# Kernel tuning notes

Measured on AMD Instinct MI355X. Metric: run time of the kernel, lower is better.

The kernel has to match this reference:

```python
import jax, jax.numpy as jnp
import numpy as np

NUM_EMBEDDINGS = 1024
EMBEDDING_DIM = 64
COMMITMENT_COST = 0.25


def setup_inputs() -> dict:
    key = jax.random.key(0)
    k1, k2 = jax.random.split(key)
    inputs = jax.random.normal(k1, (2, 64, 32, 32, 32), dtype=jnp.float32)
    embedding = jax.random.normal(k2, (NUM_EMBEDDINGS, EMBEDDING_DIM), dtype=jnp.float32)
    return {"inputs": inputs, "embedding": embedding}


def reference(inputs, embedding):
    # inputs: [B, C, D, H, W], embedding: [K, C]
    B, C, D, H, W = inputs.shape
    # flatten_permutation = [0, 2, 3, 4, 1] -> [B*D*H*W, C]
    flat_input = jnp.transpose(inputs, (0, 2, 3, 4, 1)).reshape(-1, C)
    # squared euclidean distances [N, K]
    distances = (
        jnp.sum(flat_input**2, axis=1, keepdims=True)
        + jnp.sum(embedding**2, axis=1)[None, :]
        - 2.0 * flat_input @ embedding.T
    )
    # torch.max(-distances, dim=1)[1] == argmin of distances
    encoding_indices = jnp.argmax(-distances, axis=1)  # [N]
    encoding_indices_view = encoding_indices.reshape(B, D, H, W)
    # embed: lookup then quantization_permutation [0, 4, 1, 2, 3] -> channel-first
    quantized = embedding[encoding_indices_view]            # [B, D, H, W, C]
    quantized = jnp.transpose(quantized, (0, 4, 1, 2, 3))   # [B, C, D, H, W]
    # commitment loss: MSE(stop_grad(quantized), inputs)
    loss = COMMITMENT_COST * jnp.mean((jax.lax.stop_gradient(quantized) - inputs) ** 2)
    # straight-through estimator
    quantized_st = inputs + jax.lax.stop_gradient(quantized - inputs)
    # eval path: encodings_sum = zeros(256) (hardcoded in original forward)
    encodings_sum = jnp.zeros(256, dtype=jnp.float32)
    return quantized_st, loss, encoding_indices_view, encodings_sum, embedding
```

## Files before the change

### kernel.cpp

```cpp
#include <hip/hip_runtime.h>
#include <stdint.h>

#define KCODES  1024
#define CDIM    64
#define SPATIAL 32768
#define NPOS    65536
#define NEL     4194304

#define OUT_Q    0
#define OUT_LOSS 4194304
#define OUT_IDX  4194305
#define OUT_SUM  4259841
#define OUT_EMB  4260097

#define NSET  32
#define SETB  8192
#define EIEXP 262144
#define BPOS  256

typedef _Float16 half8  __attribute__((ext_vector_type(8)));
typedef float    f32x4  __attribute__((ext_vector_type(4)));
typedef float    f32x16 __attribute__((ext_vector_type(16)));

__global__ void prep_emb(const float* __restrict__ emb, char* __restrict__ ws,
                         float* __restrict__ out) {
    int gt = blockIdx.x * 256 + threadIdx.x;
    if (gt == 0) out[OUT_LOSS] = 0.f;
    if (gt < 256) out[OUT_SUM + gt] = 0.f;
    {
        float4 v = *(const float4*)(emb + (size_t)gt * 4);
        float* o = out + OUT_EMB + (size_t)gt * 4;
        o[0] = v.x; o[1] = v.y; o[2] = v.z; o[3] = v.w;
    }
    if (gt < 8192) {
        int k = gt >> 3, oct = gt & 7;
        int set = k >> 5, row = k & 31;
        int ks = oct >> 1, hc = oct & 1;
        const float* e = emb + (size_t)k * CDIM + oct * 8;
        char* rec = ws + (size_t)set * SETB;
        _Float16* hi = (_Float16*)(rec + (ks * 2 + 0) * 1024 + (hc * 32 + row) * 16);
        _Float16* lo = (_Float16*)(rec + (ks * 2 + 1) * 1024 + (hc * 32 + row) * 16);
        float s2 = 0.f;
        half8 hv, lv;
#pragma unroll
        for (int i = 0; i < 8; ++i) {
            float v = e[i];
            s2 = fmaf(v, v, s2);
            _Float16 h = (_Float16)v;
            hv[i] = h;
            lv[i] = (_Float16)(v - (float)h);
        }
        *(half8*)hi = hv;
        *(half8*)lo = lv;
        s2 += __shfl_xor(s2, 1);
        s2 += __shfl_xor(s2, 2);
        s2 += __shfl_xor(s2, 4);
        if (oct == 0) {
            int hh = (row >> 2) & 1;
            int q  = (row & 3) | ((row >> 3) << 2);
            ((float*)(ws + EIEXP))[(set * 2 + hh) * 16 + q] = -0.5f * s2;
        }
    }
}

#define GLDS16(GSRC, LDST)                                                     \
    __builtin_amdgcn_global_load_lds(                                          \
        (const __attribute__((address_space(1))) void*)(GSRC),                 \
        (__attribute__((address_space(3))) void*)(LDST), 16, 0, 0)

__global__ __launch_bounds__(512, 2) void vq_kernel(
        const float* __restrict__ in, const float* __restrict__ emb,
        const char* __restrict__ wsA, float* __restrict__ out) {
    __shared__ __align__(16) char stg[3][SETB];
    __shared__ float xl[CDIM * 129];
    __shared__ __align__(16) float eiL[NSET * 32];
    __shared__ int   kwin[BPOS];
    __shared__ float lred[8];

    const int tid  = threadIdx.x;
    const int lane = tid & 63, wv = tid >> 6;
    const int col  = lane & 31, h = lane >> 5;
    const int p0   = blockIdx.x * BPOS;
    const int b    = p0 >> 15;
    const int s0   = p0 & 32767;
    const float* xin = in + (size_t)b * (CDIM * SPATIAL) + s0;
    const float* eiG = (const float*)(wsA + EIEXP);

    eiL[tid] = eiG[tid];
    eiL[tid + 512] = eiG[tid + 512];

    half8 bh[4], bl[4];
    for (int H = 0; H < 2; ++H) {
        {
            int p = tid & 127, cq = tid >> 7;
#pragma unroll
            for (int j = 0; j < 16; ++j) {
                int c = cq * 16 + j;
                xl[c * 129 + p] = xin[(size_t)c * SPATIAL + H * 128 + p];
            }
        }
        __syncthreads();
        if ((wv >> 2) == H) {
            int pp = (wv & 3) * 32 + col;
#pragma unroll
            for (int ks = 0; ks < 4; ++ks)
#pragma unroll
                for (int j = 0; j < 8; ++j) {
                    int c = ks * 16 + h * 8 + j;
                    float v = xl[c * 129 + pp];
                    _Float16 hh = (_Float16)v;
                    bh[ks][j] = hh;
                    bl[ks][j] = (_Float16)(v - (float)hh);
                }
        }
        __syncthreads();
    }

    GLDS16(wsA + 0 * SETB + wv * 1024 + lane * 16, &stg[0][0] + wv * 1024 + lane * 16);
    GLDS16(wsA + 1 * SETB + wv * 1024 + lane * 16, &stg[1][0] + wv * 1024 + lane * 16);

    float best = -3.402823466e38f;
    int   bk   = 0;
    char* cur = &stg[0][0];
    char* nxt = &stg[1][0];
    char* fut = &stg[2][0];
#pragma unroll 1
    for (int it = 0; it < NSET; ++it) {
        asm volatile("s_waitcnt vmcnt(1)" ::: "memory");
        __syncthreads();
        {
            int sN = (it + 2) & (NSET - 1);
            GLDS16(wsA + (size_t)sN * SETB + wv * 1024 + lane * 16,
                   fut + wv * 1024 + lane * 16);
        }
        f32x16 aA = *(const f32x16*)&eiL[(it * 2 + h) * 16];
        f32x16 aB, aC;
#pragma unroll
        for (int q = 0; q < 16; ++q) { aB[q] = 0.f; aC[q] = 0.f; }
        const char* ap = cur + (size_t)lane * 16;
#pragma unroll
        for (int ks = 0; ks < 4; ++ks) {
            half8 ah = *(const half8*)(ap + (ks * 2 + 0) * 1024);
            half8 al = *(const half8*)(ap + (ks * 2 + 1) * 1024);
            aA = __builtin_amdgcn_mfma_f32_32x32x16_f16(ah, bh[ks], aA, 0, 0, 0);
            aB = __builtin_amdgcn_mfma_f32_32x32x16_f16(ah, bl[ks], aB, 0, 0, 0);
            aC = __builtin_amdgcn_mfma_f32_32x32x16_f16(al, bh[ks], aC, 0, 0, 0);
        }
        const int kbase = it * 32 + 4 * h;
#pragma unroll
        for (int q = 0; q < 16; ++q) {
            float sc = (aA[q] + aB[q]) + aC[q];
            int   kk = kbase + (q & 3) + 8 * (q >> 2);
            if (sc > best) { best = sc; bk = kk; }
        }
        char* t0 = cur; cur = nxt; nxt = fut; fut = t0;
    }

    {
        float os = __shfl_xor(best, 32);
        int   ok = __shfl_xor(bk, 32);
        if (os > best || (os == best && ok < bk)) { best = os; bk = ok; }
        if (lane < 32) {
            kwin[wv * 32 + col] = bk;
            out[OUT_IDX + p0 + wv * 32 + col] = (float)bk;
        }
    }
    __syncthreads();

    float lsum = 0.f;
    {
        int p = tid & 255, cq = tid >> 8;
        int kk = kwin[p];
        const float* eb = emb + (size_t)kk * CDIM;
        float* q = out + OUT_Q + (size_t)b * (CDIM * SPATIAL) + s0;
#pragma unroll
        for (int j = 0; j < 32; ++j) {
            int c = cq * 32 + j;
            float x = xin[(size_t)c * SPATIAL + p];
            float e = eb[c];
            float d = e - x;
            lsum = fmaf(d, d, lsum);
            q[(size_t)c * SPATIAL + p] = x + d;
        }
    }
#pragma unroll
    for (int off = 32; off > 0; off >>= 1) lsum += __shfl_down(lsum, off);
    if (lane == 0) lred[wv] = lsum;
    __syncthreads();
    if (tid == 0) {
        float t = 0.f;
#pragma unroll
        for (int w = 0; w < 8; ++w) t += lred[w];
        atomicAdd(out + OUT_LOSS, t * (0.25f / (float)NEL));
    }
}

extern "C" void kernel_launch(void* const* d_in, const int* in_sizes, int n_in,
                              void* d_out, int out_size, void* d_ws, size_t ws_size,
                              hipStream_t stream) {
    const float* in  = (const float*)d_in[0];
    const float* emb = (const float*)d_in[1];
    float* out = (float*)d_out;
    char*  ws  = (char*)d_ws;

    prep_emb<<<64, 256, 0, stream>>>(emb, ws, out);
    vq_kernel<<<NPOS / BPOS, 512, 0, stream>>>(in, emb, ws, out);
}
```

Measured before the change: 49.04 us.

## Split codebook across wave halves with smaller position tiles and per-lane running max

Blocks now handle 128 positions instead of 256. The two groups of four waves each scan half of the codebook (16 sets) over the same 32 positions, and their candidates are merged through shared memory. The three separate MFMA accumulators are folded into one serial chain seeded with the bias. A per-accumulator-slot running max with set index replaces the per-iteration 16-way compare. The LDS footprint shrinks by reusing the staging ring for the input transpose, and launch bounds rise to 4 blocks per CU to raise occupancy, at the cost of a longer dependent MFMA chain and a cross-group merge step.

```diff
diff --git a/kernel.cpp b/kernel.cpp
--- a/kernel.cpp
+++ b/kernel.cpp
@@ -16,7 +16,8 @@
 #define NSET  32
 #define SETB  8192
 #define EIEXP 262144
-#define BPOS  256
+#define BPOS  128
+#define NRND  16
 
 typedef _Float16 half8  __attribute__((ext_vector_type(8)));
 typedef float    f32x4  __attribute__((ext_vector_type(4)));
@@ -68,114 +69,150 @@
         (const __attribute__((address_space(1))) void*)(GSRC),                 \
         (__attribute__((address_space(3))) void*)(LDST), 16, 0, 0)
 
-__global__ __launch_bounds__(512, 2) void vq_kernel(
+__global__ __launch_bounds__(512, 4) void vq_kernel(
         const float* __restrict__ in, const float* __restrict__ emb,
         const char* __restrict__ wsA, float* __restrict__ out) {
-    __shared__ __align__(16) char stg[3][SETB];
-    __shared__ float xl[CDIM * 129];
+    __shared__ __align__(16) char ring[6][SETB];
     __shared__ __align__(16) float eiL[NSET * 32];
+    __shared__ float candS[2][BPOS];
+    __shared__ int   candK[2][BPOS];
     __shared__ int   kwin[BPOS];
     __shared__ float lred[8];
 
     const int tid  = threadIdx.x;
     const int lane = tid & 63, wv = tid >> 6;
     const int col  = lane & 31, h = lane >> 5;
+    const int pg   = wv & 3, kh = wv >> 2;
     const int p0   = blockIdx.x * BPOS;
     const int b    = p0 >> 15;
     const int s0   = p0 & 32767;
     const float* xin = in + (size_t)b * (CDIM * SPATIAL) + s0;
     const float* eiG = (const float*)(wsA + EIEXP);
 
+    float* xl = (float*)&ring[0][0];
+    {
+        int p = tid & 127, cq = tid >> 7;
+#pragma unroll
+        for (int j = 0; j < 16; ++j) {
+            int c = cq * 16 + j;
+            xl[c * 129 + p] = xin[(size_t)c * SPATIAL + p];
+        }
+    }
     eiL[tid] = eiG[tid];
     eiL[tid + 512] = eiG[tid + 512];
+    __syncthreads();
 
     half8 bh[4], bl[4];
-    for (int H = 0; H < 2; ++H) {
+    {
+        int pp = pg * 32 + col;
+#pragma unroll
+        for (int ks = 0; ks < 4; ++ks)
+#pragma unroll
+            for (int j = 0; j < 8; ++j) {
+                int c = ks * 16 + h * 8 + j;
+                float v = xl[c * 129 + pp];
+                _Float16 hh = (_Float16)v;
+                bh[ks][j] = hh;
+                bl[ks][j] = (_Float16)(v - (float)hh);
+            }
+    }
+    __syncthreads();
+
+    char* sl0 = &ring[kh * 3 + 0][0];
+    char* sl1 = &ring[kh * 3 + 1][0];
+    char* sl2 = &ring[kh * 3 + 2][0];
+#define STAGE2(RSET, DST) do {                                                 \
+        const char* src_ = wsA + (size_t)(RSET) * SETB + pg * 2048 + lane * 16;\
+        char* dst_ = (DST) + pg * 2048 + lane * 16;                            \
+        GLDS16(src_, dst_);                                                    \
+        GLDS16(src_ + 1024, dst_ + 1024);                                      \
+    } while (0)
+    STAGE2(kh * 16 + 0, sl0);
+    STAGE2(kh * 16 + 1, sl1);
+    asm volatile("s_waitcnt vmcnt(2)" ::: "memory");
+    __syncthreads();
+
+    f32x16 maxS;
+    int    maxR[16];
+#pragma unroll
+    for (int q = 0; q < 16; ++q) { maxS[q] = -3.402823466e38f; maxR[q] = 0; }
+
+#pragma unroll 1
+    for (int r = 0; r < NRND; ++r) {
+        STAGE2(kh * 16 + ((r + 2) & 15), sl2);
+        const int setid = kh * 16 + r;
+        f32x16 eiv = *(const f32x16*)&eiL[(setid * 2 + h) * 16];
+        const char* ap = sl0 + (size_t)lane * 16;
+        f32x16 a;
         {
-            int p = tid & 127, cq = tid >> 7;
-#pragma unroll
-            for (int j = 0; j < 16; ++j) {
-                int c = cq * 16 + j;
-                xl[c * 129 + p] = xin[(size_t)c * SPATIAL + H * 128 + p];
-            }
-        }
+            half8 ah0 = *(const half8*)(ap);
+            half8 al0 = *(const half8*)(ap + 1024);
+            half8 ah1 = *(const half8*)(ap + 2048);
+            half8 al1 = *(const half8*)(ap + 3072);
+            half8 ah2 = *(const half8*)(ap + 4096);
+            half8 al2 = *(const half8*)(ap + 5120);
+            half8 ah3 = *(const half8*)(ap + 6144);
+            half8 al3 = *(const half8*)(ap + 7168);
+            a = __builtin_amdgcn_mfma_f32_32x32x16_f16(ah0, bh[0], eiv, 0, 0, 0);
+            a = __builtin_amdgcn_mfma_f32_32x32x16_f16(ah0, bl[0], a, 0, 0, 0);
+            a = __builtin_amdgcn_mfma_f32_32x32x16_f16(al0, bh[0], a, 0, 0, 0);
+            a = __builtin_amdgcn_mfma_f32_32x32x16_f16(ah1, bh[1], a, 0, 0, 0);
+            a = __builtin_amdgcn_mfma_f32_32x32x16_f16(ah1, bl[1], a, 0, 0, 0);
+            a = __builtin_amdgcn_mfma_f32_32x32x16_f16(al1, bh[1], a, 0, 0, 0);
+            a = __builtin_amdgcn_mfma_f32_32x32x16_f16(ah2, bh[2], a, 0, 0, 0);
+            a = __builtin_amdgcn_mfma_f32_32x32x16_f16(ah2, bl[2], a, 0, 0, 0);
+            a = __builtin_amdgcn_mfma_f32_32x32x16_f16(al2, bh[2], a, 0, 0, 0);
+            a = __builtin_amdgcn_mfma_f32_32x32x16_f16(ah3, bh[3], a, 0, 0, 0);
+            a = __builtin_amdgcn_mfma_f32_32x32x16_f16(ah3, bl[3], a, 0, 0, 0);
+            a = __builtin_amdgcn_mfma_f32_32x32x16_f16(al3, bh[3], a, 0, 0, 0);
+        }
+#pragma unroll
+        for (int q = 0; q < 16; ++q)
+            if (a[q] > maxS[q]) { maxS[q] = a[q]; maxR[q] = setid; }
+        char* t0 = sl0; sl0 = sl1; sl1 = sl2; sl2 = t0;
+        asm volatile("s_waitcnt vmcnt(2)" ::: "memory");
         __syncthreads();
-        if ((wv >> 2) == H) {
-            int pp = (wv & 3) * 32 + col;
-#pragma unroll
-            for (int ks = 0; ks < 4; ++ks)
-#pragma unroll
-                for (int j = 0; j < 8; ++j) {
-                    int c = ks * 16 + h * 8 + j;
-                    float v = xl[c * 129 + pp];
-                    _Float16 hh = (_Float16)v;
-                    bh[ks][j] = hh;
-                    bl[ks][j] = (_Float16)(v - (float)hh);
-                }
-        }
-        __syncthreads();
-    }
-
-    GLDS16(wsA + 0 * SETB + wv * 1024 + lane * 16, &stg[0][0] + wv * 1024 + lane * 16);
-    GLDS16(wsA + 1 * SETB + wv * 1024 + lane * 16, &stg[1][0] + wv * 1024 + lane * 16);
-
-    float best = -3.402823466e38f;
-    int   bk   = 0;
-    char* cur = &stg[0][0];
-    char* nxt = &stg[1][0];
-    char* fut = &stg[2][0];
-#pragma unroll 1
-    for (int it = 0; it < NSET; ++it) {
-        asm volatile("s_waitcnt vmcnt(1)" ::: "memory");
-        __syncthreads();
-        {
-            int sN = (it + 2) & (NSET - 1);
-            GLDS16(wsA + (size_t)sN * SETB + wv * 1024 + lane * 16,
-                   fut + wv * 1024 + lane * 16);
-        }
-        f32x16 aA = *(const f32x16*)&eiL[(it * 2 + h) * 16];
-        f32x16 aB, aC;
-#pragma unroll
-        for (int q = 0; q < 16; ++q) { aB[q] = 0.f; aC[q] = 0.f; }
-        const char* ap = cur + (size_t)lane * 16;
-#pragma unroll
-        for (int ks = 0; ks < 4; ++ks) {
-            half8 ah = *(const half8*)(ap + (ks * 2 + 0) * 1024);
-            half8 al = *(const half8*)(ap + (ks * 2 + 1) * 1024);
-            aA = __builtin_amdgcn_mfma_f32_32x32x16_f16(ah, bh[ks], aA, 0, 0, 0);
-            aB = __builtin_amdgcn_mfma_f32_32x32x16_f16(ah, bl[ks], aB, 0, 0, 0);
-            aC = __builtin_amdgcn_mfma_f32_32x32x16_f16(al, bh[ks], aC, 0, 0, 0);
-        }
-        const int kbase = it * 32 + 4 * h;
-#pragma unroll
-        for (int q = 0; q < 16; ++q) {
-            float sc = (aA[q] + aB[q]) + aC[q];
-            int   kk = kbase + (q & 3) + 8 * (q >> 2);
-            if (sc > best) { best = sc; bk = kk; }
-        }
-        char* t0 = cur; cur = nxt; nxt = fut; fut = t0;
-    }
-
+    }
+#undef STAGE2
+
+    float best = maxS[0];
+    int   bk   = maxR[0] * 32 + 4 * h;
+#pragma unroll
+    for (int q = 1; q < 16; ++q) {
+        float sc = maxS[q];
+        int   kk = maxR[q] * 32 + 4 * h + (q & 3) + 8 * (q >> 2);
+        if (sc > best || (sc == best && kk < bk)) { best = sc; bk = kk; }
+    }
     {
         float os = __shfl_xor(best, 32);
         int   ok = __shfl_xor(bk, 32);
         if (os > best || (os == best && ok < bk)) { best = os; bk = ok; }
-        if (lane < 32) {
-            kwin[wv * 32 + col] = bk;
-            out[OUT_IDX + p0 + wv * 32 + col] = (float)bk;
-        }
+    }
+    if (h == 0) {
+        candS[kh][pg * 32 + col] = best;
+        candK[kh][pg * 32 + col] = bk;
+    }
+    __syncthreads();
+
+    if (tid < BPOS) {
+        float s0v = candS[0][tid], s1v = candS[1][tid];
+        int   k0v = candK[0][tid], k1v = candK[1][tid];
+        int sel = (s1v > s0v) || (s1v == s0v && k1v < k0v);
+        int bkf = sel ? k1v : k0v;
+        kwin[tid] = bkf;
+        out[OUT_IDX + p0 + tid] = (float)bkf;
     }
     __syncthreads();
 
     float lsum = 0.f;
     {
-        int p = tid & 255, cq = tid >> 8;
+        int p = tid & 127, cq = tid >> 7;
         int kk = kwin[p];
         const float* eb = emb + (size_t)kk * CDIM;
         float* q = out + OUT_Q + (size_t)b * (CDIM * SPATIAL) + s0;
 #pragma unroll
-        for (int j = 0; j < 32; ++j) {
-            int c = cq * 32 + j;
+        for (int j = 0; j < 16; ++j) {
+            int c = cq * 16 + j;
             float x = xin[(size_t)c * SPATIAL + p];
             float e = eb[c];
             float d = e - x;
```

Result: faster. 42.34 us (-13.7%).
